# Performance work log

Hardware: AMD Instinct MI355X
Metric: run time of the kernel (lower is better)

Reference implementation:

```python
import jax, jax.numpy as jnp
import numpy as np

B, S, D, E, H, K = 2, 2048, 1024, 8, 4096, 2


def setup_inputs() -> dict:
    key = jax.random.key(0)
    ks = jax.random.split(key, 7)
    sd = 1.0 / np.sqrt(D)
    sh = 1.0 / np.sqrt(H)
    return {
        "x": jax.random.normal(ks[0], (B, S, D), dtype=jnp.float32),
        "router_w": jax.random.uniform(ks[1], (D, E), jnp.float32, -sd, sd),
        "router_b": jnp.zeros((E,), jnp.float32),
        "w1": jax.random.uniform(ks[2], (E, D, H), jnp.float32, -sd, sd),
        "b1": jnp.zeros((E, H), jnp.float32),
        "w2": jax.random.uniform(ks[3], (E, H, D), jnp.float32, -sh, sh),
        "b2": jnp.zeros((E, D), jnp.float32),
    }


def reference(x, router_w, router_b, w1, b1, w2, b2):
    # Router: softmax over experts, then top-k and renormalize
    router_logits = jnp.einsum("bsd,de->bse", x, router_w) + router_b
    router_probs = jax.nn.softmax(router_logits, axis=-1)
    top_k_probs, top_k_indices = jax.lax.top_k(router_probs, K)  # [B,S,K]
    top_k_probs = top_k_probs / jnp.sum(top_k_probs, axis=-1, keepdims=True)

    # Dense all-expert FFN (Block assumed: Linear -> GELU -> Linear)
    h = jax.nn.gelu(jnp.einsum("bsd,edh->bseh", x, w1) + b1)  # [B,S,E,H]
    expert_outputs = jnp.einsum("bseh,ehd->bsed", h, w2) + b2  # [B,S,E,D]

    # Gather top-k experts per token and combine with renormalized probs
    idx = top_k_indices[..., None]  # [B,S,K,1]
    selected = jnp.take_along_axis(expert_outputs, idx, axis=2)  # [B,S,K,D]
    return jnp.sum(selected * top_k_probs[..., None], axis=2)  # [B,S,D]
```

## Files before the change

kernel.cpp:

```cpp
#include <hip/hip_runtime.h>
#include <hip/hip_bf16.h>

#define TOK   4096
#define DDIM  1024
#define NEXP  8
#define HDIM  4096
#define KSEL  2
#define NPAIR (TOK * KSEL)
#define NSPLIT 4

typedef __attribute__((ext_vector_type(8))) _Float16 f16x8;
typedef __attribute__((ext_vector_type(4))) _Float16 f16x4;
typedef __attribute__((ext_vector_type(4))) float    f32x4;

__device__ __forceinline__ void gload16(const void* g, void* l) {
  __builtin_amdgcn_global_load_lds((const __attribute__((address_space(1))) void*)g,
                                   (__attribute__((address_space(3))) void*)l, 16, 0, 0);
}

__device__ __forceinline__ float gelu_tanh(float u) {
  float inner = 0.7978845608028654f * (u + 0.044715f * u * u * u);
  float t2 = __expf(2.f * inner);
  return u - u / (t2 + 1.f);
}

__global__ __launch_bounds__(256) void k_router(const float* __restrict__ x,
    const float* __restrict__ rw, const float* __restrict__ rb,
    int* __restrict__ tidx, float* __restrict__ tw,
    _Float16* __restrict__ xb) {
  const int t    = blockIdx.x * 4 + (threadIdx.x >> 6);
  const int lane = threadIdx.x & 63;
  const float* xr = x + (size_t)t * DDIM;
  _Float16*   xbr = xb + (size_t)t * DDIM;
  float acc[NEXP];
#pragma unroll
  for (int e = 0; e < NEXP; ++e) acc[e] = 0.f;
  for (int d0 = lane * 4; d0 < DDIM; d0 += 256) {
    const float4 xv = *(const float4*)(xr + d0);
    f16x4 hx;
    hx[0] = (_Float16)xv.x; hx[1] = (_Float16)xv.y;
    hx[2] = (_Float16)xv.z; hx[3] = (_Float16)xv.w;
    *(f16x4*)(xbr + d0) = hx;
#pragma unroll
    for (int i = 0; i < 4; ++i) {
      const float xs = (&xv.x)[i];
      const float4 r0 = *(const float4*)(rw + (size_t)(d0 + i) * NEXP);
      const float4 r1 = *(const float4*)(rw + (size_t)(d0 + i) * NEXP + 4);
      acc[0] += xs * r0.x; acc[1] += xs * r0.y; acc[2] += xs * r0.z; acc[3] += xs * r0.w;
      acc[4] += xs * r1.x; acc[5] += xs * r1.y; acc[6] += xs * r1.z; acc[7] += xs * r1.w;
    }
  }
#pragma unroll
  for (int e = 0; e < NEXP; ++e) {
    float v = acc[e];
#pragma unroll
    for (int s = 32; s; s >>= 1) v += __shfl_xor(v, s, 64);
    acc[e] = v;
  }
  if (lane == 0) {
    float lg[NEXP];
#pragma unroll
    for (int e = 0; e < NEXP; ++e) lg[e] = acc[e] + rb[e];
    int i0 = 0;
#pragma unroll
    for (int e = 1; e < NEXP; ++e) if (lg[e] > lg[i0]) i0 = e;
    int i1 = -1; float best = -3.4e38f;
#pragma unroll
    for (int e = 0; e < NEXP; ++e) {
      if (e == i0) continue;
      if (lg[e] > best) { best = lg[e]; i1 = e; }
    }
    float w0 = 1.f / (1.f + expf(lg[i1] - lg[i0]));
    tidx[t * 2]     = i0;  tidx[t * 2 + 1] = i1;
    tw[t * 2]       = w0;  tw[t * 2 + 1]   = 1.f - w0;
  }
}

__global__ __launch_bounds__(1024) void k_scan(const int* __restrict__ tidx,
                       const float* __restrict__ tw,
                       int* __restrict__ offs,
                       int* __restrict__ row_token, float* __restrict__ row_w,
                       int* __restrict__ inv) {
  __shared__ int hist[NEXP];
  __shared__ int soff[NEXP + 1];
  __shared__ int scur[NEXP];
  if (threadIdx.x < NEXP) hist[threadIdx.x] = 0;
  __syncthreads();
  const int lane = threadIdx.x & 63;
  int e_loc[NPAIR / 1024];
#pragma unroll
  for (int it = 0; it < NPAIR / 1024; ++it) {
    const int p = it * 1024 + threadIdx.x;
    const int e = tidx[p];
    e_loc[it] = e;
#pragma unroll
    for (int ee = 0; ee < NEXP; ++ee) {
      unsigned long long m = __ballot(e == ee);
      if (m && lane == 0) atomicAdd(&hist[ee], __popcll(m));
    }
  }
  __syncthreads();
  if (threadIdx.x == 0) {
    int run = 0;
    for (int e = 0; e < NEXP; ++e) { soff[e] = run; scur[e] = run; run += hist[e]; }
    soff[NEXP] = run;
    for (int e = 0; e <= NEXP; ++e) offs[e] = soff[e];
  }
  __syncthreads();
#pragma unroll
  for (int it = 0; it < NPAIR / 1024; ++it) {
    const int p = it * 1024 + threadIdx.x;
    const int e = e_loc[it];
    int pos = 0;
#pragma unroll
    for (int ee = 0; ee < NEXP; ++ee) {
      unsigned long long m = __ballot(e == ee);
      if (!m) continue;
      int base = 0;
      if (lane == 0) base = atomicAdd(&scur[ee], __popcll(m));
      base = __shfl(base, 0, 64);
      if (e == ee) pos = base + __popcll(m & ((1ull << lane) - 1ull));
    }
    row_token[pos] = p >> 1;
    row_w[pos]     = tw[p];
    inv[p]         = pos;
  }
}

__global__ __launch_bounds__(256) void k_transpose2(const float* __restrict__ w1,
    const float* __restrict__ w2, _Float16* __restrict__ w1t, _Float16* __restrict__ w2t) {
  __shared__ _Float16 tile[64][72];
  const int zz = blockIdx.y;
  const float* ip; _Float16* op; int Rr, Cc, i0, j0;
  if (zz < NEXP) {
    ip = w1 + (size_t)zz * DDIM * HDIM;  op = w1t + (size_t)zz * DDIM * HDIM;
    Rr = DDIM; Cc = HDIM;
    i0 = (blockIdx.x >> 6) * 64; j0 = (blockIdx.x & 63) * 64;
  } else {
    ip = w2 + (size_t)(zz - NEXP) * HDIM * DDIM;  op = w2t + (size_t)(zz - NEXP) * HDIM * DDIM;
    Rr = HDIM; Cc = DDIM;
    i0 = (blockIdx.x >> 4) * 64; j0 = (blockIdx.x & 15) * 64;
  }
  const int tx = threadIdx.x & 15, ty = threadIdx.x >> 4;
#pragma unroll
  for (int rr = 0; rr < 4; ++rr) {
    int r = ty + rr * 16;
    float4 v = *(const float4*)(ip + (size_t)(i0 + r) * Cc + j0 + tx * 4);
    tile[r][tx * 4 + 0] = (_Float16)v.x;
    tile[r][tx * 4 + 1] = (_Float16)v.y;
    tile[r][tx * 4 + 2] = (_Float16)v.z;
    tile[r][tx * 4 + 3] = (_Float16)v.w;
  }
  __syncthreads();
#pragma unroll
  for (int cc = 0; cc < 4; ++cc) {
    int c = ty + cc * 16;
    f16x4 o;
#pragma unroll
    for (int k = 0; k < 4; ++k) o[k] = tile[tx * 4 + k][c];
    *(f16x4*)(op + (size_t)(j0 + c) * Rr + i0 + tx * 4) = o;
  }
}

#define BM 128
#define BN 128
#define BKK 32


__global__ __launch_bounds__(256) void k_gemm1(
    const _Float16* __restrict__ xb,
    const _Float16* __restrict__ w1t,
    const float* __restrict__ b1,
    const int* __restrict__ offs,
    const int* __restrict__ row_token,
    _Float16* __restrict__ hbuf) {
  const int e    = blockIdx.z;
  const int off0 = offs[e];
  const int ne   = offs[e + 1] - off0;
  const int m0   = blockIdx.y * BM;
  if (m0 >= ne) return;
  const int n0   = blockIdx.x * BN;
  const int mrem = ne - m0;

  __shared__ __align__(16) char smem[32768];

  const int tid = threadIdx.x;
  const int wv = tid >> 6, lane = tid & 63;
  const int l15 = lane & 15;
  const int wr = wv >> 1, wc = wv & 1;

  const int rA0 = (wv * 2 + 0) * 16 + (lane >> 2);
  const int rA1 = (wv * 2 + 1) * 16 + (lane >> 2);
  const char* a_c = (const char*)xb;
  const char* b_c = (const char*)(w1t + (size_t)e * HDIM * DDIM);
  const int rc0 = (rA0 < mrem) ? rA0 : (mrem - 1);
  const int rc1 = (rA1 < mrem) ? rA1 : (mrem - 1);
  const char* ap0 = a_c + (size_t)row_token[off0 + m0 + rc0] * (DDIM * 2)
                        + (((lane & 3) ^ ((rA0 >> 1) & 3)) << 4);
  const char* ap1 = a_c + (size_t)row_token[off0 + m0 + rc1] * (DDIM * 2)
                        + (((lane & 3) ^ ((rA1 >> 1) & 3)) << 4);
  const char* bp0 = b_c + (size_t)(n0 + rA0) * (DDIM * 2)
                        + (((lane & 3) ^ ((rA0 >> 1) & 3)) << 4);
  const char* bp1 = b_c + (size_t)(n0 + rA1) * (DDIM * 2)
                        + (((lane & 3) ^ ((rA1 >> 1) & 3)) << 4);
  char* ldsA0 = smem + (wv * 2 + 0) * 1024;
  char* ldsA1 = smem + (wv * 2 + 1) * 1024;
  char* ldsB0 = smem + 16384 + (wv * 2 + 0) * 1024;
  char* ldsB1 = smem + 16384 + (wv * 2 + 1) * 1024;

  const unsigned foff = (unsigned)(((lane >> 4) ^ ((l15 >> 1) & 3)) << 4);

  f32x4 acc[4][4] = {};
  const int NT = DDIM / BKK;

  gload16(ap0, ldsA0); gload16(ap1, ldsA1);
  gload16(bp0, ldsB0); gload16(bp1, ldsB1);
  asm volatile("s_waitcnt vmcnt(0)" ::: "memory");
  __builtin_amdgcn_s_barrier();

#pragma unroll 2
  for (int ks = 0; ks < NT; ++ks) {
    const int cur = ks & 1;
    if (ks + 1 < NT) {
      const int nb = (cur ^ 1) * 8192;
      const size_t kb = (size_t)(ks + 1) * 64;
      gload16(ap0 + kb, ldsA0 + nb); gload16(ap1 + kb, ldsA1 + nb);
      gload16(bp0 + kb, ldsB0 + nb); gload16(bp1 + kb, ldsB1 + nb);
    }
    const char* Ab = smem + cur * 8192;
    const char* Bb = smem + 16384 + cur * 8192;
    f16x8 af[4], bfr[4];
#pragma unroll
    for (int m = 0; m < 4; ++m)
      af[m] = *(const f16x8*)(Ab + (wr * 64 + m * 16 + l15) * 64 + foff);
#pragma unroll
    for (int n = 0; n < 4; ++n)
      bfr[n] = *(const f16x8*)(Bb + (wc * 64 + n * 16 + l15) * 64 + foff);
#pragma unroll
    for (int m = 0; m < 4; ++m)
#pragma unroll
      for (int n = 0; n < 4; ++n)
        acc[m][n] = __builtin_amdgcn_mfma_f32_16x16x32_f16(af[m], bfr[n], acc[m][n], 0, 0, 0);
    __builtin_amdgcn_sched_barrier(0);
    asm volatile("s_waitcnt vmcnt(0)" ::: "memory");
    __builtin_amdgcn_s_barrier();
  }

  float bias[4];
#pragma unroll
  for (int n = 0; n < 4; ++n)
    bias[n] = b1[(size_t)e * HDIM + n0 + wc * 64 + n * 16 + l15];
#pragma unroll
  for (int m = 0; m < 4; ++m) {
#pragma unroll
    for (int j = 0; j < 4; ++j) {
      int row = wr * 64 + m * 16 + (lane >> 4) * 4 + j;
#pragma unroll
      for (int n = 0; n < 4; ++n) {
        int col = wc * 64 + n * 16 + l15;
        *(_Float16*)(smem + (row << 8) + (((col << 1) ^ ((row & 15) << 4)))) =
            (_Float16)gelu_tanh(acc[m][n][j] + bias[n]);
      }
    }
  }
  __syncthreads();
  {
    const int srow = tid >> 1, half = tid & 1;
    if (srow < mrem) {
      _Float16* hr = hbuf + (size_t)(off0 + m0 + srow) * HDIM + n0 + half * 64;
#pragma unroll
      for (int i = 0; i < 8; ++i) {
        f16x8 v = *(const f16x8*)(smem + (srow << 8) + (((half * 128 + i * 16) ^ ((srow & 15) << 4))));
        *(f16x8*)(hr + i * 8) = v;
      }
    }
  }
}

template <bool YB>
__global__ __launch_bounds__(256) void k_gemm2(
    const _Float16* __restrict__ hbuf,
    const _Float16* __restrict__ w2t,
    const float* __restrict__ b2,
    const int* __restrict__ offs,
    const int* __restrict__ row_token,
    const float* __restrict__ row_w,
    _Float16* __restrict__ yb,
    float* __restrict__ out) {
  const int zz = blockIdx.z;
  const int e  = zz >> 2;
  const int kh = zz & 3;
  const int off0 = offs[e];
  const int ne   = offs[e + 1] - off0;
  const int m0   = blockIdx.y * BM;
  if (m0 >= ne) return;
  const int n0   = blockIdx.x * BN;
  const int mrem = ne - m0;

  __shared__ __align__(16) char smem[32768];

  const int tid = threadIdx.x;
  const int wv = tid >> 6, lane = tid & 63;
  const int l15 = lane & 15;
  const int wr = wv >> 1, wc = wv & 1;

  const int rA0 = (wv * 2 + 0) * 16 + (lane >> 2);
  const int rA1 = (wv * 2 + 1) * 16 + (lane >> 2);
  const char* a_c = (const char*)hbuf;
  const char* b_c = (const char*)(w2t + (size_t)e * DDIM * HDIM);
  const int rc0 = (rA0 < mrem) ? rA0 : (mrem - 1);
  const int rc1 = (rA1 < mrem) ? rA1 : (mrem - 1);
  const size_t khb = (size_t)kh * ((HDIM / NSPLIT) * 2);
  const char* ap0 = a_c + (size_t)(off0 + m0 + rc0) * (HDIM * 2) + khb
                        + (((lane & 3) ^ ((rA0 >> 1) & 3)) << 4);
  const char* ap1 = a_c + (size_t)(off0 + m0 + rc1) * (HDIM * 2) + khb
                        + (((lane & 3) ^ ((rA1 >> 1) & 3)) << 4);
  const char* bp0 = b_c + (size_t)(n0 + rA0) * (HDIM * 2) + khb
                        + (((lane & 3) ^ ((rA0 >> 1) & 3)) << 4);
  const char* bp1 = b_c + (size_t)(n0 + rA1) * (HDIM * 2) + khb
                        + (((lane & 3) ^ ((rA1 >> 1) & 3)) << 4);
  char* ldsA0 = smem + (wv * 2 + 0) * 1024;
  char* ldsA1 = smem + (wv * 2 + 1) * 1024;
  char* ldsB0 = smem + 16384 + (wv * 2 + 0) * 1024;
  char* ldsB1 = smem + 16384 + (wv * 2 + 1) * 1024;

  const unsigned foff = (unsigned)(((lane >> 4) ^ ((l15 >> 1) & 3)) << 4);

  f32x4 acc[4][4] = {};
  const int NT = (HDIM / NSPLIT) / BKK;

  gload16(ap0, ldsA0); gload16(ap1, ldsA1);
  gload16(bp0, ldsB0); gload16(bp1, ldsB1);
  asm volatile("s_waitcnt vmcnt(0)" ::: "memory");
  __builtin_amdgcn_s_barrier();

#pragma unroll 2
  for (int ks = 0; ks < NT; ++ks) {
    const int cur = ks & 1;
    if (ks + 1 < NT) {
      const int nb = (cur ^ 1) * 8192;
      const size_t kb = (size_t)(ks + 1) * 64;
      gload16(ap0 + kb, ldsA0 + nb); gload16(ap1 + kb, ldsA1 + nb);
      gload16(bp0 + kb, ldsB0 + nb); gload16(bp1 + kb, ldsB1 + nb);
    }
    const char* Ab = smem + cur * 8192;
    const char* Bb = smem + 16384 + cur * 8192;
    f16x8 af[4], bfr[4];
#pragma unroll
    for (int m = 0; m < 4; ++m)
      af[m] = *(const f16x8*)(Ab + (wr * 64 + m * 16 + l15) * 64 + foff);
#pragma unroll
    for (int n = 0; n < 4; ++n)
      bfr[n] = *(const f16x8*)(Bb + (wc * 64 + n * 16 + l15) * 64 + foff);
#pragma unroll
    for (int m = 0; m < 4; ++m)
#pragma unroll
      for (int n = 0; n < 4; ++n)
        acc[m][n] = __builtin_amdgcn_mfma_f32_16x16x32_f16(af[m], bfr[n], acc[m][n], 0, 0, 0);
    __builtin_amdgcn_sched_barrier(0);
    asm volatile("s_waitcnt vmcnt(0)" ::: "memory");
    __builtin_amdgcn_s_barrier();
  }

  if (YB) {
    _Float16* ypart = yb + (size_t)kh * NPAIR * DDIM;
#pragma unroll
    for (int m = 0; m < 4; ++m) {
#pragma unroll
      for (int j = 0; j < 4; ++j) {
        int row = wr * 64 + m * 16 + (lane >> 4) * 4 + j;
#pragma unroll
        for (int n = 0; n < 4; ++n) {
          int col = wc * 64 + n * 16 + l15;
          *(_Float16*)(smem + (row << 8) + (((col << 1) ^ ((row & 15) << 4)))) =
              (_Float16)acc[m][n][j];
        }
      }
    }
    __syncthreads();
    const int srow = tid >> 1, half = tid & 1;
    if (srow < mrem) {
      _Float16* yr = ypart + (size_t)(off0 + m0 + srow) * DDIM + n0 + half * 64;
#pragma unroll
      for (int i = 0; i < 8; ++i) {
        f16x8 v = *(const f16x8*)(smem + (srow << 8) + (((half * 128 + i * 16) ^ ((srow & 15) << 4))));
        *(f16x8*)(yr + i * 8) = v;
      }
    }
  } else {
    float bias[4];
#pragma unroll
    for (int n = 0; n < 4; ++n)
      bias[n] = (kh == 0) ? b2[(size_t)e * DDIM + n0 + wc * 64 + n * 16 + l15] : 0.f;
#pragma unroll
    for (int m = 0; m < 4; ++m) {
#pragma unroll
      for (int j = 0; j < 4; ++j) {
        int row = wr * 64 + m * 16 + (lane >> 4) * 4 + j;
        if (row < mrem) {
          int g = off0 + m0 + row;
          float wgt = row_w[g];
          float* op = out + (size_t)row_token[g] * DDIM + n0 + wc * 64 + l15;
#pragma unroll
          for (int n = 0; n < 4; ++n)
            atomicAdd(op + n * 16, wgt * (acc[m][n][j] + bias[n]));
        }
      }
    }
  }
}

__global__ __launch_bounds__(256) void k_combine(const _Float16* __restrict__ yb,
    const int* __restrict__ inv, const int* __restrict__ tidx,
    const float* __restrict__ tw, const float* __restrict__ b2,
    float* __restrict__ out) {
  const int t  = blockIdx.x * 2 + (threadIdx.x >> 7);
  const int c8 = (threadIdx.x & 127) * 8;
  const int g0 = inv[2 * t],  g1 = inv[2 * t + 1];
  const int e0 = tidx[2 * t], e1 = tidx[2 * t + 1];
  const float w0 = tw[2 * t], w1 = tw[2 * t + 1];
  float s0[8] = {0,0,0,0,0,0,0,0}, s1[8] = {0,0,0,0,0,0,0,0};
#pragma unroll
  for (int p = 0; p < NSPLIT; ++p) {
    const _Float16* yp = yb + (size_t)p * NPAIR * DDIM;
    f16x8 a = *(const f16x8*)(yp + (size_t)g0 * DDIM + c8);
    f16x8 b = *(const f16x8*)(yp + (size_t)g1 * DDIM + c8);
#pragma unroll
    for (int i = 0; i < 8; ++i) { s0[i] += (float)a[i]; s1[i] += (float)b[i]; }
  }
  float o[8];
#pragma unroll
  for (int i = 0; i < 8; ++i) {
    float bA = b2[(size_t)e0 * DDIM + c8 + i];
    float bB = b2[(size_t)e1 * DDIM + c8 + i];
    o[i] = w0 * (s0[i] + bA) + w1 * (s1[i] + bB);
  }
  float* op = out + (size_t)t * DDIM + c8;
  *(float4*)op       = make_float4(o[0], o[1], o[2], o[3]);
  *(float4*)(op + 4) = make_float4(o[4], o[5], o[6], o[7]);
}

extern "C" void kernel_launch(void* const* d_in, const int* in_sizes, int n_in,
                              void* d_out, int out_size, void* d_ws, size_t ws_size,
                              hipStream_t stream) {
  const float* x  = (const float*)d_in[0];
  const float* rw = (const float*)d_in[1];
  const float* rb = (const float*)d_in[2];
  const float* w1 = (const float*)d_in[3];
  const float* b1 = (const float*)d_in[4];
  const float* w2 = (const float*)d_in[5];
  const float* b2 = (const float*)d_in[6];
  float* out = (float*)d_out;
  char* ws = (char*)d_ws;

  int*      tidx    = (int*)(ws + 0);
  float*    tw      = (float*)(ws + 32768);
  int*      offs    = (int*)(ws + 65792);
  int*      row_tok = (int*)(ws + 66048);
  float*    row_w   = (float*)(ws + 98816);
  int*      inv     = (int*)(ws + 131584);
  _Float16* xb      = (_Float16*)(ws + 164352);
  _Float16* wtA     = (_Float16*)(ws + 8552960);
  _Float16* wtB     = (_Float16*)(ws + 75661824);
  _Float16* hb      = (_Float16*)(ws + 142770688);
  _Float16* yb      = wtA;
  const bool big = ws_size >= 209879552ULL;

  if (!big) hipMemsetAsync(out, 0, (size_t)TOK * DDIM * sizeof(float), stream);

  k_router<<<dim3(TOK / 4), 256, 0, stream>>>(x, rw, rb, tidx, tw, xb);
  k_scan<<<dim3(1), 1024, 0, stream>>>(tidx, tw, offs, row_tok, row_w, inv);
  k_transpose2<<<dim3(1024, 2 * NEXP), 256, 0, stream>>>(w1, w2, wtA, wtB);
  k_gemm1<<<dim3(HDIM / BN, TOK / BM, NEXP), 256, 0, stream>>>(xb, wtA, b1, offs, row_tok, hb);
  if (big) {
    k_gemm2<true><<<dim3(DDIM / BN, TOK / BM, NEXP * NSPLIT), 256, 0, stream>>>(
        hb, wtB, b2, offs, row_tok, row_w, yb, out);
    k_combine<<<dim3(TOK / 2), 256, 0, stream>>>(yb, inv, tidx, tw, b2, out);
  } else {
    k_gemm2<false><<<dim3(DDIM / BN, TOK / BM, NEXP * NSPLIT), 256, 0, stream>>>(
        hb, wtB, b2, offs, row_tok, row_w, yb, out);
  }
}
```

Measured before the change: 385.5 us.

## Replace double-buffered BK=32 loop with single-buffered BK=64 tiles in both GEMMs

Both expert GEMM kernels drop the double-buffered K=32 pipeline, where the next tile's global-to-LDS load was issued before computing the current one. They now use a single-buffered K=64 tile with a new 8-way XOR swizzle, and each thread issues four 16-byte loads per operand per step. This halves the number of K iterations and barriers per tile, but global loads no longer overlap with MFMA work inside a block. The design relies on other resident blocks to hide load latency, which exposes memory latency if occupancy is low.

```diff
diff --git a/kernel.cpp b/kernel.cpp
--- a/kernel.cpp
+++ b/kernel.cpp
@@ -164,7 +164,7 @@
 
 #define BM 128
 #define BN 128
-#define BKK 32
+#define BK 64
 
 
 __global__ __launch_bounds__(256) void k_gemm1(
@@ -183,67 +183,56 @@
   const int mrem = ne - m0;
 
   __shared__ __align__(16) char smem[32768];
+  char* As = smem;
+  char* Bs = smem + 16384;
 
   const int tid = threadIdx.x;
   const int wv = tid >> 6, lane = tid & 63;
   const int l15 = lane & 15;
   const int wr = wv >> 1, wc = wv & 1;
-
-  const int rA0 = (wv * 2 + 0) * 16 + (lane >> 2);
-  const int rA1 = (wv * 2 + 1) * 16 + (lane >> 2);
+  const int lr = lane >> 3;
+  const unsigned ssl = (unsigned)(((lane & 7) ^ lr) << 4);
+
   const char* a_c = (const char*)xb;
   const char* b_c = (const char*)(w1t + (size_t)e * HDIM * DDIM);
-  const int rc0 = (rA0 < mrem) ? rA0 : (mrem - 1);
-  const int rc1 = (rA1 < mrem) ? rA1 : (mrem - 1);
-  const char* ap0 = a_c + (size_t)row_token[off0 + m0 + rc0] * (DDIM * 2)
-                        + (((lane & 3) ^ ((rA0 >> 1) & 3)) << 4);
-  const char* ap1 = a_c + (size_t)row_token[off0 + m0 + rc1] * (DDIM * 2)
-                        + (((lane & 3) ^ ((rA1 >> 1) & 3)) << 4);
-  const char* bp0 = b_c + (size_t)(n0 + rA0) * (DDIM * 2)
-                        + (((lane & 3) ^ ((rA0 >> 1) & 3)) << 4);
-  const char* bp1 = b_c + (size_t)(n0 + rA1) * (DDIM * 2)
-                        + (((lane & 3) ^ ((rA1 >> 1) & 3)) << 4);
-  char* ldsA0 = smem + (wv * 2 + 0) * 1024;
-  char* ldsA1 = smem + (wv * 2 + 1) * 1024;
-  char* ldsB0 = smem + 16384 + (wv * 2 + 0) * 1024;
-  char* ldsB1 = smem + 16384 + (wv * 2 + 1) * 1024;
-
-  const unsigned foff = (unsigned)(((lane >> 4) ^ ((l15 >> 1) & 3)) << 4);
+
+  size_t apB[4], bpB[4];
+#pragma unroll
+  for (int i = 0; i < 4; ++i) {
+    int r  = wv * 32 + i * 8 + lr;
+    int rc = (r < mrem) ? r : (mrem - 1);
+    apB[i] = (size_t)row_token[off0 + m0 + rc] * (DDIM * 2) + ssl;
+    bpB[i] = (size_t)(n0 + r) * (DDIM * 2) + ssl;
+  }
 
   f32x4 acc[4][4] = {};
-  const int NT = DDIM / BKK;
-
-  gload16(ap0, ldsA0); gload16(ap1, ldsA1);
-  gload16(bp0, ldsB0); gload16(bp1, ldsB1);
-  asm volatile("s_waitcnt vmcnt(0)" ::: "memory");
-  __builtin_amdgcn_s_barrier();
-
-#pragma unroll 2
+  const int NT = DDIM / BK;
+
   for (int ks = 0; ks < NT; ++ks) {
-    const int cur = ks & 1;
-    if (ks + 1 < NT) {
-      const int nb = (cur ^ 1) * 8192;
-      const size_t kb = (size_t)(ks + 1) * 64;
-      gload16(ap0 + kb, ldsA0 + nb); gload16(ap1 + kb, ldsA1 + nb);
-      gload16(bp0 + kb, ldsB0 + nb); gload16(bp1 + kb, ldsB1 + nb);
-    }
-    const char* Ab = smem + cur * 8192;
-    const char* Bb = smem + 16384 + cur * 8192;
-    f16x8 af[4], bfr[4];
-#pragma unroll
-    for (int m = 0; m < 4; ++m)
-      af[m] = *(const f16x8*)(Ab + (wr * 64 + m * 16 + l15) * 64 + foff);
-#pragma unroll
-    for (int n = 0; n < 4; ++n)
-      bfr[n] = *(const f16x8*)(Bb + (wc * 64 + n * 16 + l15) * 64 + foff);
-#pragma unroll
-    for (int m = 0; m < 4; ++m)
+    const size_t kb = (size_t)ks * 128;
+#pragma unroll
+    for (int i = 0; i < 4; ++i) {
+      gload16(a_c + apB[i] + kb, As + (wv * 32 + i * 8) * 128);
+      gload16(b_c + bpB[i] + kb, Bs + (wv * 32 + i * 8) * 128);
+    }
+    __syncthreads();
+#pragma unroll
+    for (int kk = 0; kk < 2; ++kk) {
+      f16x8 af[4], bfr[4];
+      const unsigned rsl = (unsigned)((kk * 4 + (lane >> 4)) ^ (l15 & 7)) << 4;
+#pragma unroll
+      for (int m = 0; m < 4; ++m)
+        af[m] = *(const f16x8*)(As + (wr * 64 + m * 16 + l15) * 128 + rsl);
 #pragma unroll
       for (int n = 0; n < 4; ++n)
-        acc[m][n] = __builtin_amdgcn_mfma_f32_16x16x32_f16(af[m], bfr[n], acc[m][n], 0, 0, 0);
-    __builtin_amdgcn_sched_barrier(0);
-    asm volatile("s_waitcnt vmcnt(0)" ::: "memory");
-    __builtin_amdgcn_s_barrier();
+        bfr[n] = *(const f16x8*)(Bs + (wc * 64 + n * 16 + l15) * 128 + rsl);
+#pragma unroll
+      for (int m = 0; m < 4; ++m)
+#pragma unroll
+        for (int n = 0; n < 4; ++n)
+          acc[m][n] = __builtin_amdgcn_mfma_f32_16x16x32_f16(af[m], bfr[n], acc[m][n], 0, 0, 0);
+    }
+    __syncthreads();
   }
 
   float bias[4];
@@ -298,68 +287,57 @@
   const int mrem = ne - m0;
 
   __shared__ __align__(16) char smem[32768];
+  char* As = smem;
+  char* Bs = smem + 16384;
 
   const int tid = threadIdx.x;
   const int wv = tid >> 6, lane = tid & 63;
   const int l15 = lane & 15;
   const int wr = wv >> 1, wc = wv & 1;
-
-  const int rA0 = (wv * 2 + 0) * 16 + (lane >> 2);
-  const int rA1 = (wv * 2 + 1) * 16 + (lane >> 2);
+  const int lr = lane >> 3;
+  const unsigned ssl = (unsigned)(((lane & 7) ^ lr) << 4);
+
   const char* a_c = (const char*)hbuf;
   const char* b_c = (const char*)(w2t + (size_t)e * DDIM * HDIM);
-  const int rc0 = (rA0 < mrem) ? rA0 : (mrem - 1);
-  const int rc1 = (rA1 < mrem) ? rA1 : (mrem - 1);
   const size_t khb = (size_t)kh * ((HDIM / NSPLIT) * 2);
-  const char* ap0 = a_c + (size_t)(off0 + m0 + rc0) * (HDIM * 2) + khb
-                        + (((lane & 3) ^ ((rA0 >> 1) & 3)) << 4);
-  const char* ap1 = a_c + (size_t)(off0 + m0 + rc1) * (HDIM * 2) + khb
-                        + (((lane & 3) ^ ((rA1 >> 1) & 3)) << 4);
-  const char* bp0 = b_c + (size_t)(n0 + rA0) * (HDIM * 2) + khb
-                        + (((lane & 3) ^ ((rA0 >> 1) & 3)) << 4);
-  const char* bp1 = b_c + (size_t)(n0 + rA1) * (HDIM * 2) + khb
-                        + (((lane & 3) ^ ((rA1 >> 1) & 3)) << 4);
-  char* ldsA0 = smem + (wv * 2 + 0) * 1024;
-  char* ldsA1 = smem + (wv * 2 + 1) * 1024;
-  char* ldsB0 = smem + 16384 + (wv * 2 + 0) * 1024;
-  char* ldsB1 = smem + 16384 + (wv * 2 + 1) * 1024;
-
-  const unsigned foff = (unsigned)(((lane >> 4) ^ ((l15 >> 1) & 3)) << 4);
+
+  size_t apB[4], bpB[4];
+#pragma unroll
+  for (int i = 0; i < 4; ++i) {
+    int r  = wv * 32 + i * 8 + lr;
+    int rc = (r < mrem) ? r : (mrem - 1);
+    apB[i] = (size_t)(off0 + m0 + rc) * (HDIM * 2) + khb + ssl;
+    bpB[i] = (size_t)(n0 + r) * (HDIM * 2) + khb + ssl;
+  }
 
   f32x4 acc[4][4] = {};
-  const int NT = (HDIM / NSPLIT) / BKK;
-
-  gload16(ap0, ldsA0); gload16(ap1, ldsA1);
-  gload16(bp0, ldsB0); gload16(bp1, ldsB1);
-  asm volatile("s_waitcnt vmcnt(0)" ::: "memory");
-  __builtin_amdgcn_s_barrier();
-
-#pragma unroll 2
+  const int NT = (HDIM / NSPLIT) / BK;
+
   for (int ks = 0; ks < NT; ++ks) {
-    const int cur = ks & 1;
-    if (ks + 1 < NT) {
-      const int nb = (cur ^ 1) * 8192;
-      const size_t kb = (size_t)(ks + 1) * 64;
-      gload16(ap0 + kb, ldsA0 + nb); gload16(ap1 + kb, ldsA1 + nb);
-      gload16(bp0 + kb, ldsB0 + nb); gload16(bp1 + kb, ldsB1 + nb);
-    }
-    const char* Ab = smem + cur * 8192;
-    const char* Bb = smem + 16384 + cur * 8192;
-    f16x8 af[4], bfr[4];
-#pragma unroll
-    for (int m = 0; m < 4; ++m)
-      af[m] = *(const f16x8*)(Ab + (wr * 64 + m * 16 + l15) * 64 + foff);
-#pragma unroll
-    for (int n = 0; n < 4; ++n)
-      bfr[n] = *(const f16x8*)(Bb + (wc * 64 + n * 16 + l15) * 64 + foff);
-#pragma unroll
-    for (int m = 0; m < 4; ++m)
+    const size_t kb = (size_t)ks * 128;
+#pragma unroll
+    for (int i = 0; i < 4; ++i) {
+      gload16(a_c + apB[i] + kb, As + (wv * 32 + i * 8) * 128);
+      gload16(b_c + bpB[i] + kb, Bs + (wv * 32 + i * 8) * 128);
+    }
+    __syncthreads();
+#pragma unroll
+    for (int kk = 0; kk < 2; ++kk) {
+      f16x8 af[4], bfr[4];
+      const unsigned rsl = (unsigned)((kk * 4 + (lane >> 4)) ^ (l15 & 7)) << 4;
+#pragma unroll
+      for (int m = 0; m < 4; ++m)
+        af[m] = *(const f16x8*)(As + (wr * 64 + m * 16 + l15) * 128 + rsl);
 #pragma unroll
       for (int n = 0; n < 4; ++n)
-        acc[m][n] = __builtin_amdgcn_mfma_f32_16x16x32_f16(af[m], bfr[n], acc[m][n], 0, 0, 0);
-    __builtin_amdgcn_sched_barrier(0);
-    asm volatile("s_waitcnt vmcnt(0)" ::: "memory");
-    __builtin_amdgcn_s_barrier();
+        bfr[n] = *(const f16x8*)(Bs + (wc * 64 + n * 16 + l15) * 128 + rsl);
+#pragma unroll
+      for (int m = 0; m < 4; ++m)
+#pragma unroll
+        for (int n = 0; n < 4; ++n)
+          acc[m][n] = __builtin_amdgcn_mfma_f32_16x16x32_f16(af[m], bfr[n], acc[m][n], 0, 0, 0);
+    }
+    __syncthreads();
   }
 
   if (YB) {
```

Result: slower. 400.5 us (+3.9%).

## Use 2-wave 128x128 GEMM blocks with 64x128 warp tiles and async prefetch wait

Applied to the files above, without the earlier changes.

Both expert GEMM kernels drop from four waves to two per 128x128 tile. Each wave now computes a 64x128 sub-tile with 32 accumulators and issues four global-to-LDS loads per operand. The wait on the next tile's loads is moved to the top of the iteration with vmcnt(8), so the prefetch for the following stage stays in flight during the MFMAs instead of being drained at the end of the loop. This aims to raise MFMA work per LDS fragment load and improve load/compute overlap. It costs twice the accumulator registers per wave and halves the threads per block, which may lower occupancy and latency hiding.

```diff
diff --git a/kernel.cpp b/kernel.cpp
--- a/kernel.cpp
+++ b/kernel.cpp
@@ -167,7 +167,7 @@
 #define BKK 32
 
 
-__global__ __launch_bounds__(256) void k_gemm1(
+__global__ __launch_bounds__(128) void k_gemm1(
     const _Float16* __restrict__ xb,
     const _Float16* __restrict__ w1t,
     const float* __restrict__ b1,
@@ -187,36 +187,31 @@
   const int tid = threadIdx.x;
   const int wv = tid >> 6, lane = tid & 63;
   const int l15 = lane & 15;
-  const int wr = wv >> 1, wc = wv & 1;
-
-  const int rA0 = (wv * 2 + 0) * 16 + (lane >> 2);
-  const int rA1 = (wv * 2 + 1) * 16 + (lane >> 2);
+
   const char* a_c = (const char*)xb;
   const char* b_c = (const char*)(w1t + (size_t)e * HDIM * DDIM);
-  const int rc0 = (rA0 < mrem) ? rA0 : (mrem - 1);
-  const int rc1 = (rA1 < mrem) ? rA1 : (mrem - 1);
-  const char* ap0 = a_c + (size_t)row_token[off0 + m0 + rc0] * (DDIM * 2)
-                        + (((lane & 3) ^ ((rA0 >> 1) & 3)) << 4);
-  const char* ap1 = a_c + (size_t)row_token[off0 + m0 + rc1] * (DDIM * 2)
-                        + (((lane & 3) ^ ((rA1 >> 1) & 3)) << 4);
-  const char* bp0 = b_c + (size_t)(n0 + rA0) * (DDIM * 2)
-                        + (((lane & 3) ^ ((rA0 >> 1) & 3)) << 4);
-  const char* bp1 = b_c + (size_t)(n0 + rA1) * (DDIM * 2)
-                        + (((lane & 3) ^ ((rA1 >> 1) & 3)) << 4);
-  char* ldsA0 = smem + (wv * 2 + 0) * 1024;
-  char* ldsA1 = smem + (wv * 2 + 1) * 1024;
-  char* ldsB0 = smem + 16384 + (wv * 2 + 0) * 1024;
-  char* ldsB1 = smem + 16384 + (wv * 2 + 1) * 1024;
+
+  size_t apB[4], bpB[4];
+  char *ldsA[4], *ldsB[4];
+#pragma unroll
+  for (int i = 0; i < 4; ++i) {
+    const int c = wv * 4 + i;
+    const int r = c * 16 + (lane >> 2);
+    const int rc = (r < mrem) ? r : (mrem - 1);
+    const unsigned so = (unsigned)(((lane & 3) ^ ((r >> 1) & 3)) << 4);
+    apB[i] = (size_t)row_token[off0 + m0 + rc] * (DDIM * 2) + so;
+    bpB[i] = (size_t)(n0 + r) * (DDIM * 2) + so;
+    ldsA[i] = smem + c * 1024;
+    ldsB[i] = smem + 16384 + c * 1024;
+  }
 
   const unsigned foff = (unsigned)(((lane >> 4) ^ ((l15 >> 1) & 3)) << 4);
 
-  f32x4 acc[4][4] = {};
+  f32x4 acc[4][8] = {};
   const int NT = DDIM / BKK;
 
-  gload16(ap0, ldsA0); gload16(ap1, ldsA1);
-  gload16(bp0, ldsB0); gload16(bp1, ldsB1);
-  asm volatile("s_waitcnt vmcnt(0)" ::: "memory");
-  __builtin_amdgcn_s_barrier();
+#pragma unroll
+  for (int i = 0; i < 4; ++i) { gload16(a_c + apB[i], ldsA[i]); gload16(b_c + bpB[i], ldsB[i]); }
 
 #pragma unroll 2
   for (int ks = 0; ks < NT; ++ks) {
@@ -224,40 +219,47 @@
     if (ks + 1 < NT) {
       const int nb = (cur ^ 1) * 8192;
       const size_t kb = (size_t)(ks + 1) * 64;
-      gload16(ap0 + kb, ldsA0 + nb); gload16(ap1 + kb, ldsA1 + nb);
-      gload16(bp0 + kb, ldsB0 + nb); gload16(bp1 + kb, ldsB1 + nb);
-    }
+#pragma unroll
+      for (int i = 0; i < 4; ++i) {
+        gload16(a_c + apB[i] + kb, ldsA[i] + nb);
+        gload16(b_c + bpB[i] + kb, ldsB[i] + nb);
+      }
+      asm volatile("s_waitcnt vmcnt(8)" ::: "memory");
+    } else {
+      asm volatile("s_waitcnt vmcnt(0)" ::: "memory");
+    }
+    __builtin_amdgcn_sched_barrier(0);
+    __builtin_amdgcn_s_barrier();
     const char* Ab = smem + cur * 8192;
     const char* Bb = smem + 16384 + cur * 8192;
-    f16x8 af[4], bfr[4];
+    f16x8 af[4], bfr[8];
 #pragma unroll
     for (int m = 0; m < 4; ++m)
-      af[m] = *(const f16x8*)(Ab + (wr * 64 + m * 16 + l15) * 64 + foff);
-#pragma unroll
-    for (int n = 0; n < 4; ++n)
-      bfr[n] = *(const f16x8*)(Bb + (wc * 64 + n * 16 + l15) * 64 + foff);
+      af[m] = *(const f16x8*)(Ab + (wv * 64 + m * 16 + l15) * 64 + foff);
+#pragma unroll
+    for (int n = 0; n < 8; ++n)
+      bfr[n] = *(const f16x8*)(Bb + (n * 16 + l15) * 64 + foff);
 #pragma unroll
     for (int m = 0; m < 4; ++m)
 #pragma unroll
-      for (int n = 0; n < 4; ++n)
+      for (int n = 0; n < 8; ++n)
         acc[m][n] = __builtin_amdgcn_mfma_f32_16x16x32_f16(af[m], bfr[n], acc[m][n], 0, 0, 0);
     __builtin_amdgcn_sched_barrier(0);
-    asm volatile("s_waitcnt vmcnt(0)" ::: "memory");
     __builtin_amdgcn_s_barrier();
   }
 
-  float bias[4];
-#pragma unroll
-  for (int n = 0; n < 4; ++n)
-    bias[n] = b1[(size_t)e * HDIM + n0 + wc * 64 + n * 16 + l15];
+  float bias[8];
+#pragma unroll
+  for (int n = 0; n < 8; ++n)
+    bias[n] = b1[(size_t)e * HDIM + n0 + n * 16 + l15];
 #pragma unroll
   for (int m = 0; m < 4; ++m) {
 #pragma unroll
     for (int j = 0; j < 4; ++j) {
-      int row = wr * 64 + m * 16 + (lane >> 4) * 4 + j;
-#pragma unroll
-      for (int n = 0; n < 4; ++n) {
-        int col = wc * 64 + n * 16 + l15;
+      int row = wv * 64 + m * 16 + (lane >> 4) * 4 + j;
+#pragma unroll
+      for (int n = 0; n < 8; ++n) {
+        int col = n * 16 + l15;
         *(_Float16*)(smem + (row << 8) + (((col << 1) ^ ((row & 15) << 4)))) =
             (_Float16)gelu_tanh(acc[m][n][j] + bias[n]);
       }
@@ -265,12 +267,12 @@
   }
   __syncthreads();
   {
-    const int srow = tid >> 1, half = tid & 1;
+    const int srow = tid;
     if (srow < mrem) {
-      _Float16* hr = hbuf + (size_t)(off0 + m0 + srow) * HDIM + n0 + half * 64;
-#pragma unroll
-      for (int i = 0; i < 8; ++i) {
-        f16x8 v = *(const f16x8*)(smem + (srow << 8) + (((half * 128 + i * 16) ^ ((srow & 15) << 4))));
+      _Float16* hr = hbuf + (size_t)(off0 + m0 + srow) * HDIM + n0;
+#pragma unroll
+      for (int i = 0; i < 16; ++i) {
+        f16x8 v = *(const f16x8*)(smem + (srow << 8) + (((i * 16) ^ ((srow & 15) << 4))));
         *(f16x8*)(hr + i * 8) = v;
       }
     }
@@ -278,7 +280,7 @@
 }
 
 template <bool YB>
-__global__ __launch_bounds__(256) void k_gemm2(
+__global__ __launch_bounds__(128) void k_gemm2(
     const _Float16* __restrict__ hbuf,
     const _Float16* __restrict__ w2t,
     const float* __restrict__ b2,
@@ -302,37 +304,32 @@
   const int tid = threadIdx.x;
   const int wv = tid >> 6, lane = tid & 63;
   const int l15 = lane & 15;
-  const int wr = wv >> 1, wc = wv & 1;
-
-  const int rA0 = (wv * 2 + 0) * 16 + (lane >> 2);
-  const int rA1 = (wv * 2 + 1) * 16 + (lane >> 2);
+
   const char* a_c = (const char*)hbuf;
   const char* b_c = (const char*)(w2t + (size_t)e * DDIM * HDIM);
-  const int rc0 = (rA0 < mrem) ? rA0 : (mrem - 1);
-  const int rc1 = (rA1 < mrem) ? rA1 : (mrem - 1);
   const size_t khb = (size_t)kh * ((HDIM / NSPLIT) * 2);
-  const char* ap0 = a_c + (size_t)(off0 + m0 + rc0) * (HDIM * 2) + khb
-                        + (((lane & 3) ^ ((rA0 >> 1) & 3)) << 4);
-  const char* ap1 = a_c + (size_t)(off0 + m0 + rc1) * (HDIM * 2) + khb
-                        + (((lane & 3) ^ ((rA1 >> 1) & 3)) << 4);
-  const char* bp0 = b_c + (size_t)(n0 + rA0) * (HDIM * 2) + khb
-                        + (((lane & 3) ^ ((rA0 >> 1) & 3)) << 4);
-  const char* bp1 = b_c + (size_t)(n0 + rA1) * (HDIM * 2) + khb
-                        + (((lane & 3) ^ ((rA1 >> 1) & 3)) << 4);
-  char* ldsA0 = smem + (wv * 2 + 0) * 1024;
-  char* ldsA1 = smem + (wv * 2 + 1) * 1024;
-  char* ldsB0 = smem + 16384 + (wv * 2 + 0) * 1024;
-  char* ldsB1 = smem + 16384 + (wv * 2 + 1) * 1024;
+
+  size_t apB[4], bpB[4];
+  char *ldsA[4], *ldsB[4];
+#pragma unroll
+  for (int i = 0; i < 4; ++i) {
+    const int c = wv * 4 + i;
+    const int r = c * 16 + (lane >> 2);
+    const int rc = (r < mrem) ? r : (mrem - 1);
+    const unsigned so = (unsigned)(((lane & 3) ^ ((r >> 1) & 3)) << 4);
+    apB[i] = (size_t)(off0 + m0 + rc) * (HDIM * 2) + khb + so;
+    bpB[i] = (size_t)(n0 + r) * (HDIM * 2) + khb + so;
+    ldsA[i] = smem + c * 1024;
+    ldsB[i] = smem + 16384 + c * 1024;
+  }
 
   const unsigned foff = (unsigned)(((lane >> 4) ^ ((l15 >> 1) & 3)) << 4);
 
-  f32x4 acc[4][4] = {};
+  f32x4 acc[4][8] = {};
   const int NT = (HDIM / NSPLIT) / BKK;
 
-  gload16(ap0, ldsA0); gload16(ap1, ldsA1);
-  gload16(bp0, ldsB0); gload16(bp1, ldsB1);
-  asm volatile("s_waitcnt vmcnt(0)" ::: "memory");
-  __builtin_amdgcn_s_barrier();
+#pragma unroll
+  for (int i = 0; i < 4; ++i) { gload16(a_c + apB[i], ldsA[i]); gload16(b_c + bpB[i], ldsB[i]); }
 
 #pragma unroll 2
   for (int ks = 0; ks < NT; ++ks) {
@@ -340,25 +337,32 @@
     if (ks + 1 < NT) {
       const int nb = (cur ^ 1) * 8192;
       const size_t kb = (size_t)(ks + 1) * 64;
-      gload16(ap0 + kb, ldsA0 + nb); gload16(ap1 + kb, ldsA1 + nb);
-      gload16(bp0 + kb, ldsB0 + nb); gload16(bp1 + kb, ldsB1 + nb);
-    }
+#pragma unroll
+      for (int i = 0; i < 4; ++i) {
+        gload16(a_c + apB[i] + kb, ldsA[i] + nb);
+        gload16(b_c + bpB[i] + kb, ldsB[i] + nb);
+      }
+      asm volatile("s_waitcnt vmcnt(8)" ::: "memory");
+    } else {
+      asm volatile("s_waitcnt vmcnt(0)" ::: "memory");
+    }
+    __builtin_amdgcn_sched_barrier(0);
+    __builtin_amdgcn_s_barrier();
     const char* Ab = smem + cur * 8192;
     const char* Bb = smem + 16384 + cur * 8192;
-    f16x8 af[4], bfr[4];
+    f16x8 af[4], bfr[8];
 #pragma unroll
     for (int m = 0; m < 4; ++m)
-      af[m] = *(const f16x8*)(Ab + (wr * 64 + m * 16 + l15) * 64 + foff);
-#pragma unroll
-    for (int n = 0; n < 4; ++n)
-      bfr[n] = *(const f16x8*)(Bb + (wc * 64 + n * 16 + l15) * 64 + foff);
+      af[m] = *(const f16x8*)(Ab + (wv * 64 + m * 16 + l15) * 64 + foff);
+#pragma unroll
+    for (int n = 0; n < 8; ++n)
+      bfr[n] = *(const f16x8*)(Bb + (n * 16 + l15) * 64 + foff);
 #pragma unroll
     for (int m = 0; m < 4; ++m)
 #pragma unroll
-      for (int n = 0; n < 4; ++n)
+      for (int n = 0; n < 8; ++n)
         acc[m][n] = __builtin_amdgcn_mfma_f32_16x16x32_f16(af[m], bfr[n], acc[m][n], 0, 0, 0);
     __builtin_amdgcn_sched_barrier(0);
-    asm volatile("s_waitcnt vmcnt(0)" ::: "memory");
     __builtin_amdgcn_s_barrier();
   }
 
@@ -368,41 +372,41 @@
     for (int m = 0; m < 4; ++m) {
 #pragma unroll
       for (int j = 0; j < 4; ++j) {
-        int row = wr * 64 + m * 16 + (lane >> 4) * 4 + j;
-#pragma unroll
-        for (int n = 0; n < 4; ++n) {
-          int col = wc * 64 + n * 16 + l15;
+        int row = wv * 64 + m * 16 + (lane >> 4) * 4 + j;
+#pragma unroll
+        for (int n = 0; n < 8; ++n) {
+          int col = n * 16 + l15;
           *(_Float16*)(smem + (row << 8) + (((col << 1) ^ ((row & 15) << 4)))) =
               (_Float16)acc[m][n][j];
         }
       }
     }
     __syncthreads();
-    const int srow = tid >> 1, half = tid & 1;
+    const int srow = tid;
     if (srow < mrem) {
-      _Float16* yr = ypart + (size_t)(off0 + m0 + srow) * DDIM + n0 + half * 64;
-#pragma unroll
-      for (int i = 0; i < 8; ++i) {
-        f16x8 v = *(const f16x8*)(smem + (srow << 8) + (((half * 128 + i * 16) ^ ((srow & 15) << 4))));
+      _Float16* yr = ypart + (size_t)(off0 + m0 + srow) * DDIM + n0;
+#pragma unroll
+      for (int i = 0; i < 16; ++i) {
+        f16x8 v = *(const f16x8*)(smem + (srow << 8) + (((i * 16) ^ ((srow & 15) << 4))));
         *(f16x8*)(yr + i * 8) = v;
       }
     }
   } else {
-    float bias[4];
-#pragma unroll
-    for (int n = 0; n < 4; ++n)
-      bias[n] = (kh == 0) ? b2[(size_t)e * DDIM + n0 + wc * 64 + n * 16 + l15] : 0.f;
+    float bias[8];
+#pragma unroll
+    for (int n = 0; n < 8; ++n)
+      bias[n] = (kh == 0) ? b2[(size_t)e * DDIM + n0 + n * 16 + l15] : 0.f;
 #pragma unroll
     for (int m = 0; m < 4; ++m) {
 #pragma unroll
       for (int j = 0; j < 4; ++j) {
-        int row = wr * 64 + m * 16 + (lane >> 4) * 4 + j;
+        int row = wv * 64 + m * 16 + (lane >> 4) * 4 + j;
         if (row < mrem) {
           int g = off0 + m0 + row;
           float wgt = row_w[g];
-          float* op = out + (size_t)row_token[g] * DDIM + n0 + wc * 64 + l15;
-#pragma unroll
-          for (int n = 0; n < 4; ++n)
+          float* op = out + (size_t)row_token[g] * DDIM + n0 + l15;
+#pragma unroll
+          for (int n = 0; n < 8; ++n)
             atomicAdd(op + n * 16, wgt * (acc[m][n][j] + bias[n]));
         }
       }
@@ -471,13 +475,13 @@
   k_router<<<dim3(TOK / 4), 256, 0, stream>>>(x, rw, rb, tidx, tw, xb);
   k_scan<<<dim3(1), 1024, 0, stream>>>(tidx, tw, offs, row_tok, row_w, inv);
   k_transpose2<<<dim3(1024, 2 * NEXP), 256, 0, stream>>>(w1, w2, wtA, wtB);
-  k_gemm1<<<dim3(HDIM / BN, TOK / BM, NEXP), 256, 0, stream>>>(xb, wtA, b1, offs, row_tok, hb);
+  k_gemm1<<<dim3(HDIM / BN, TOK / BM, NEXP), 128, 0, stream>>>(xb, wtA, b1, offs, row_tok, hb);
   if (big) {
-    k_gemm2<true><<<dim3(DDIM / BN, TOK / BM, NEXP * NSPLIT), 256, 0, stream>>>(
+    k_gemm2<true><<<dim3(DDIM / BN, TOK / BM, NEXP * NSPLIT), 128, 0, stream>>>(
         hb, wtB, b2, offs, row_tok, row_w, yb, out);
     k_combine<<<dim3(TOK / 2), 256, 0, stream>>>(yb, inv, tidx, tw, b2, out);
   } else {
-    k_gemm2<false><<<dim3(DDIM / BN, TOK / BM, NEXP * NSPLIT), 256, 0, stream>>>(
+    k_gemm2<false><<<dim3(DDIM / BN, TOK / BM, NEXP * NSPLIT), 128, 0, stream>>>(
         hb, wtB, b2, offs, row_tok, row_w, yb, out);
   }
 }
```

Result: slower. 441.5 us (+14.5%).

## Enlarge gemm2 tile to 256x128, halve split-K, and refine pipeline waits

Applied to the files above, without the earlier changes.

The down-projection GEMM now uses a 256x128 block tile, each wave computing 64x128 from shared B fragments, and the split-K factor drops from 4 to 2. This cuts the number of blocks, the partial-sum traffic and the work in the combine kernel. Both GEMMs move the wait-and-barrier before compute and use a partial vmcnt so the prefetch of the next K-tile overlaps the current one. The trade-offs are higher register pressure from 128 accumulators, larger LDS use, and fewer blocks for load balancing across experts. The grid's y dimension also changes to NPAIR/256.

```diff
diff --git a/kernel.cpp b/kernel.cpp
--- a/kernel.cpp
+++ b/kernel.cpp
@@ -7,7 +7,7 @@
 #define HDIM  4096
 #define KSEL  2
 #define NPAIR (TOK * KSEL)
-#define NSPLIT 4
+#define NSPLIT 2
 
 typedef __attribute__((ext_vector_type(8))) _Float16 f16x8;
 typedef __attribute__((ext_vector_type(4))) _Float16 f16x4;
@@ -165,7 +165,6 @@
 #define BM 128
 #define BN 128
 #define BKK 32
-
 
 __global__ __launch_bounds__(256) void k_gemm1(
     const _Float16* __restrict__ xb,
@@ -215,8 +214,6 @@
 
   gload16(ap0, ldsA0); gload16(ap1, ldsA1);
   gload16(bp0, ldsB0); gload16(bp1, ldsB1);
-  asm volatile("s_waitcnt vmcnt(0)" ::: "memory");
-  __builtin_amdgcn_s_barrier();
 
 #pragma unroll 2
   for (int ks = 0; ks < NT; ++ks) {
@@ -226,7 +223,12 @@
       const size_t kb = (size_t)(ks + 1) * 64;
       gload16(ap0 + kb, ldsA0 + nb); gload16(ap1 + kb, ldsA1 + nb);
       gload16(bp0 + kb, ldsB0 + nb); gload16(bp1 + kb, ldsB1 + nb);
-    }
+      asm volatile("s_waitcnt vmcnt(4)" ::: "memory");
+    } else {
+      asm volatile("s_waitcnt vmcnt(0)" ::: "memory");
+    }
+    __builtin_amdgcn_sched_barrier(0);
+    __builtin_amdgcn_s_barrier();
     const char* Ab = smem + cur * 8192;
     const char* Bb = smem + 16384 + cur * 8192;
     f16x8 af[4], bfr[4];
@@ -242,7 +244,6 @@
       for (int n = 0; n < 4; ++n)
         acc[m][n] = __builtin_amdgcn_mfma_f32_16x16x32_f16(af[m], bfr[n], acc[m][n], 0, 0, 0);
     __builtin_amdgcn_sched_barrier(0);
-    asm volatile("s_waitcnt vmcnt(0)" ::: "memory");
     __builtin_amdgcn_s_barrier();
   }
 
@@ -278,7 +279,7 @@
 }
 
 template <bool YB>
-__global__ __launch_bounds__(256) void k_gemm2(
+__global__ __launch_bounds__(256, 2) void k_gemm2(
     const _Float16* __restrict__ hbuf,
     const _Float16* __restrict__ w2t,
     const float* __restrict__ b2,
@@ -288,121 +289,138 @@
     _Float16* __restrict__ yb,
     float* __restrict__ out) {
   const int zz = blockIdx.z;
-  const int e  = zz >> 2;
-  const int kh = zz & 3;
+  const int e  = zz >> 1;
+  const int kh = zz & 1;
   const int off0 = offs[e];
   const int ne   = offs[e + 1] - off0;
-  const int m0   = blockIdx.y * BM;
+  const int m0   = blockIdx.y * 256;
   if (m0 >= ne) return;
-  const int n0   = blockIdx.x * BN;
+  const int n0   = blockIdx.x * 128;
   const int mrem = ne - m0;
 
-  __shared__ __align__(16) char smem[32768];
+  __shared__ __align__(16) char smem[49152];
 
   const int tid = threadIdx.x;
   const int wv = tid >> 6, lane = tid & 63;
   const int l15 = lane & 15;
-  const int wr = wv >> 1, wc = wv & 1;
-
-  const int rA0 = (wv * 2 + 0) * 16 + (lane >> 2);
-  const int rA1 = (wv * 2 + 1) * 16 + (lane >> 2);
+
   const char* a_c = (const char*)hbuf;
   const char* b_c = (const char*)(w2t + (size_t)e * DDIM * HDIM);
-  const int rc0 = (rA0 < mrem) ? rA0 : (mrem - 1);
-  const int rc1 = (rA1 < mrem) ? rA1 : (mrem - 1);
-  const size_t khb = (size_t)kh * ((HDIM / NSPLIT) * 2);
-  const char* ap0 = a_c + (size_t)(off0 + m0 + rc0) * (HDIM * 2) + khb
-                        + (((lane & 3) ^ ((rA0 >> 1) & 3)) << 4);
-  const char* ap1 = a_c + (size_t)(off0 + m0 + rc1) * (HDIM * 2) + khb
-                        + (((lane & 3) ^ ((rA1 >> 1) & 3)) << 4);
-  const char* bp0 = b_c + (size_t)(n0 + rA0) * (HDIM * 2) + khb
-                        + (((lane & 3) ^ ((rA0 >> 1) & 3)) << 4);
-  const char* bp1 = b_c + (size_t)(n0 + rA1) * (HDIM * 2) + khb
-                        + (((lane & 3) ^ ((rA1 >> 1) & 3)) << 4);
-  char* ldsA0 = smem + (wv * 2 + 0) * 1024;
-  char* ldsA1 = smem + (wv * 2 + 1) * 1024;
-  char* ldsB0 = smem + 16384 + (wv * 2 + 0) * 1024;
-  char* ldsB1 = smem + 16384 + (wv * 2 + 1) * 1024;
+  const size_t khb = (size_t)kh * (2048 * 2);
+
+  size_t apB[4]; size_t bpB[2];
+  char* ldsA[4]; char* ldsB[2];
+#pragma unroll
+  for (int i = 0; i < 4; ++i) {
+    const int c = wv * 4 + i;
+    const int r = c * 16 + (lane >> 2);
+    const int rc = (r < mrem) ? r : (mrem - 1);
+    const unsigned so = (unsigned)(((lane & 3) ^ ((r >> 1) & 3)) << 4);
+    apB[i] = (size_t)(off0 + m0 + rc) * (HDIM * 2) + khb + so;
+    ldsA[i] = smem + c * 1024;
+  }
+#pragma unroll
+  for (int i = 0; i < 2; ++i) {
+    const int c = wv * 2 + i;
+    const int r = c * 16 + (lane >> 2);
+    const unsigned so = (unsigned)(((lane & 3) ^ ((r >> 1) & 3)) << 4);
+    bpB[i] = (size_t)(n0 + r) * (HDIM * 2) + khb + so;
+    ldsB[i] = smem + 32768 + c * 1024;
+  }
 
   const unsigned foff = (unsigned)(((lane >> 4) ^ ((l15 >> 1) & 3)) << 4);
 
-  f32x4 acc[4][4] = {};
-  const int NT = (HDIM / NSPLIT) / BKK;
-
-  gload16(ap0, ldsA0); gload16(ap1, ldsA1);
-  gload16(bp0, ldsB0); gload16(bp1, ldsB1);
-  asm volatile("s_waitcnt vmcnt(0)" ::: "memory");
-  __builtin_amdgcn_s_barrier();
+  f32x4 acc[4][8] = {};
+  const int NT = 2048 / BKK;
+
+#pragma unroll
+  for (int i = 0; i < 4; ++i) gload16(a_c + apB[i], ldsA[i]);
+#pragma unroll
+  for (int i = 0; i < 2; ++i) gload16(b_c + bpB[i], ldsB[i]);
 
 #pragma unroll 2
   for (int ks = 0; ks < NT; ++ks) {
     const int cur = ks & 1;
     if (ks + 1 < NT) {
-      const int nb = (cur ^ 1) * 8192;
       const size_t kb = (size_t)(ks + 1) * 64;
-      gload16(ap0 + kb, ldsA0 + nb); gload16(ap1 + kb, ldsA1 + nb);
-      gload16(bp0 + kb, ldsB0 + nb); gload16(bp1 + kb, ldsB1 + nb);
-    }
-    const char* Ab = smem + cur * 8192;
-    const char* Bb = smem + 16384 + cur * 8192;
-    f16x8 af[4], bfr[4];
+      const int nbA = (cur ^ 1) * 16384;
+      const int nbB = (cur ^ 1) * 8192;
+#pragma unroll
+      for (int i = 0; i < 4; ++i) gload16(a_c + apB[i] + kb, ldsA[i] + nbA);
+#pragma unroll
+      for (int i = 0; i < 2; ++i) gload16(b_c + bpB[i] + kb, ldsB[i] + nbB);
+      asm volatile("s_waitcnt vmcnt(6)" ::: "memory");
+    } else {
+      asm volatile("s_waitcnt vmcnt(0)" ::: "memory");
+    }
+    __builtin_amdgcn_sched_barrier(0);
+    __builtin_amdgcn_s_barrier();
+    const char* Ab = smem + cur * 16384;
+    const char* Bb = smem + 32768 + cur * 8192;
+    f16x8 af[4], bfr[8];
 #pragma unroll
     for (int m = 0; m < 4; ++m)
-      af[m] = *(const f16x8*)(Ab + (wr * 64 + m * 16 + l15) * 64 + foff);
-#pragma unroll
-    for (int n = 0; n < 4; ++n)
-      bfr[n] = *(const f16x8*)(Bb + (wc * 64 + n * 16 + l15) * 64 + foff);
+      af[m] = *(const f16x8*)(Ab + (wv * 64 + m * 16 + l15) * 64 + foff);
+#pragma unroll
+    for (int n = 0; n < 8; ++n)
+      bfr[n] = *(const f16x8*)(Bb + (n * 16 + l15) * 64 + foff);
 #pragma unroll
     for (int m = 0; m < 4; ++m)
 #pragma unroll
-      for (int n = 0; n < 4; ++n)
+      for (int n = 0; n < 8; ++n)
         acc[m][n] = __builtin_amdgcn_mfma_f32_16x16x32_f16(af[m], bfr[n], acc[m][n], 0, 0, 0);
     __builtin_amdgcn_sched_barrier(0);
-    asm volatile("s_waitcnt vmcnt(0)" ::: "memory");
     __builtin_amdgcn_s_barrier();
   }
 
   if (YB) {
     _Float16* ypart = yb + (size_t)kh * NPAIR * DDIM;
 #pragma unroll
-    for (int m = 0; m < 4; ++m) {
-#pragma unroll
-      for (int j = 0; j < 4; ++j) {
-        int row = wr * 64 + m * 16 + (lane >> 4) * 4 + j;
-#pragma unroll
-        for (int n = 0; n < 4; ++n) {
-          int col = wc * 64 + n * 16 + l15;
-          *(_Float16*)(smem + (row << 8) + (((col << 1) ^ ((row & 15) << 4)))) =
-              (_Float16)acc[m][n][j];
+    for (int p = 0; p < 2; ++p) {
+      if ((wv >> 1) == p) {
+#pragma unroll
+        for (int m = 0; m < 4; ++m) {
+#pragma unroll
+          for (int j = 0; j < 4; ++j) {
+            int lrow = (wv & 1) * 64 + m * 16 + (lane >> 4) * 4 + j;
+#pragma unroll
+            for (int n = 0; n < 8; ++n) {
+              int col = n * 16 + l15;
+              *(_Float16*)(smem + (lrow << 8) + (((col << 1) ^ ((lrow & 15) << 4)))) =
+                  (_Float16)acc[m][n][j];
+            }
+          }
         }
       }
-    }
-    __syncthreads();
-    const int srow = tid >> 1, half = tid & 1;
-    if (srow < mrem) {
-      _Float16* yr = ypart + (size_t)(off0 + m0 + srow) * DDIM + n0 + half * 64;
-#pragma unroll
-      for (int i = 0; i < 8; ++i) {
-        f16x8 v = *(const f16x8*)(smem + (srow << 8) + (((half * 128 + i * 16) ^ ((srow & 15) << 4))));
-        *(f16x8*)(yr + i * 8) = v;
+      __syncthreads();
+      const int srow = tid >> 1, half = tid & 1;
+      const int grow = p * 128 + srow;
+      if (grow < mrem) {
+        _Float16* yr = ypart + (size_t)(off0 + m0 + grow) * DDIM + n0 + half * 64;
+#pragma unroll
+        for (int i = 0; i < 8; ++i) {
+          f16x8 v = *(const f16x8*)(smem + (srow << 8) + (((half * 128 + i * 16) ^ ((srow & 15) << 4))));
+          *(f16x8*)(yr + i * 8) = v;
+        }
       }
+      __syncthreads();
     }
   } else {
-    float bias[4];
-#pragma unroll
-    for (int n = 0; n < 4; ++n)
-      bias[n] = (kh == 0) ? b2[(size_t)e * DDIM + n0 + wc * 64 + n * 16 + l15] : 0.f;
+    float bias[8];
+#pragma unroll
+    for (int n = 0; n < 8; ++n)
+      bias[n] = (kh == 0) ? b2[(size_t)e * DDIM + n0 + n * 16 + l15] : 0.f;
 #pragma unroll
     for (int m = 0; m < 4; ++m) {
 #pragma unroll
       for (int j = 0; j < 4; ++j) {
-        int row = wr * 64 + m * 16 + (lane >> 4) * 4 + j;
+        int row = wv * 64 + m * 16 + (lane >> 4) * 4 + j;
         if (row < mrem) {
           int g = off0 + m0 + row;
           float wgt = row_w[g];
-          float* op = out + (size_t)row_token[g] * DDIM + n0 + wc * 64 + l15;
-#pragma unroll
-          for (int n = 0; n < 4; ++n)
+          float* op = out + (size_t)row_token[g] * DDIM + n0 + l15;
+#pragma unroll
+          for (int n = 0; n < 8; ++n)
             atomicAdd(op + n * 16, wgt * (acc[m][n][j] + bias[n]));
         }
       }
@@ -419,21 +437,17 @@
   const int g0 = inv[2 * t],  g1 = inv[2 * t + 1];
   const int e0 = tidx[2 * t], e1 = tidx[2 * t + 1];
   const float w0 = tw[2 * t], w1 = tw[2 * t + 1];
-  float s0[8] = {0,0,0,0,0,0,0,0}, s1[8] = {0,0,0,0,0,0,0,0};
-#pragma unroll
-  for (int p = 0; p < NSPLIT; ++p) {
-    const _Float16* yp = yb + (size_t)p * NPAIR * DDIM;
-    f16x8 a = *(const f16x8*)(yp + (size_t)g0 * DDIM + c8);
-    f16x8 b = *(const f16x8*)(yp + (size_t)g1 * DDIM + c8);
-#pragma unroll
-    for (int i = 0; i < 8; ++i) { s0[i] += (float)a[i]; s1[i] += (float)b[i]; }
-  }
+  const _Float16* y1p = yb + (size_t)NPAIR * DDIM;
+  f16x8 a0 = *(const f16x8*)(yb  + (size_t)g0 * DDIM + c8);
+  f16x8 a1 = *(const f16x8*)(y1p + (size_t)g0 * DDIM + c8);
+  f16x8 b0 = *(const f16x8*)(yb  + (size_t)g1 * DDIM + c8);
+  f16x8 b1v = *(const f16x8*)(y1p + (size_t)g1 * DDIM + c8);
   float o[8];
 #pragma unroll
   for (int i = 0; i < 8; ++i) {
     float bA = b2[(size_t)e0 * DDIM + c8 + i];
     float bB = b2[(size_t)e1 * DDIM + c8 + i];
-    o[i] = w0 * (s0[i] + bA) + w1 * (s1[i] + bB);
+    o[i] = w0 * ((float)a0[i] + (float)a1[i] + bA) + w1 * ((float)b0[i] + (float)b1v[i] + bB);
   }
   float* op = out + (size_t)t * DDIM + c8;
   *(float4*)op       = make_float4(o[0], o[1], o[2], o[3]);
@@ -473,11 +487,11 @@
   k_transpose2<<<dim3(1024, 2 * NEXP), 256, 0, stream>>>(w1, w2, wtA, wtB);
   k_gemm1<<<dim3(HDIM / BN, TOK / BM, NEXP), 256, 0, stream>>>(xb, wtA, b1, offs, row_tok, hb);
   if (big) {
-    k_gemm2<true><<<dim3(DDIM / BN, TOK / BM, NEXP * NSPLIT), 256, 0, stream>>>(
+    k_gemm2<true><<<dim3(DDIM / 128, NPAIR / 256, NEXP * NSPLIT), 256, 0, stream>>>(
         hb, wtB, b2, offs, row_tok, row_w, yb, out);
     k_combine<<<dim3(TOK / 2), 256, 0, stream>>>(yb, inv, tidx, tw, b2, out);
   } else {
-    k_gemm2<false><<<dim3(DDIM / BN, TOK / BM, NEXP * NSPLIT), 256, 0, stream>>>(
+    k_gemm2<false><<<dim3(DDIM / 128, NPAIR / 256, NEXP * NSPLIT), 256, 0, stream>>>(
         hb, wtB, b2, offs, row_tok, row_w, yb, out);
   }
 }
```

Result: faster. 356.2 us (-7.6%).
